# Kernel tuning notes

Measured on AMD Instinct MI355X. Metric: run time of the kernel, lower is better.

The kernel has to match this reference:

```python
import jax, jax.numpy as jnp
import numpy as np

N = 100000
E = 1600000
IN_C = 128
HID = 32
HEADS = 4
OUT_C = 16
G = 128
NEG_SLOPE = 0.2


def setup_inputs() -> dict:
    key = jax.random.key(0)
    ks = jax.random.split(key, 16)
    x = jax.random.normal(ks[0], (N, IN_C), dtype=jnp.float32)
    edge_index = jax.random.randint(ks[1], (2, E), 0, N, dtype=jnp.int64)
    batch = jnp.sort(jax.random.randint(ks[2], (N,), 0, G, dtype=jnp.int64))
    node_weights = jax.random.uniform(ks[3], (N, 1), dtype=jnp.float32)
    s = 1.0 / np.sqrt(IN_C)
    W1 = jax.random.uniform(ks[4], (IN_C, HEADS * HID), jnp.float32, -s, s)
    att_src1 = jax.random.uniform(ks[5], (HEADS, HID), jnp.float32, -s, s)
    att_dst1 = jax.random.uniform(ks[6], (HEADS, HID), jnp.float32, -s, s)
    b1 = jnp.zeros((HEADS * HID,), jnp.float32)
    s2 = 1.0 / np.sqrt(HEADS * HID)
    W2 = jax.random.uniform(ks[7], (HEADS * HID, HID), jnp.float32, -s2, s2)
    att_src2 = jax.random.uniform(ks[8], (1, HID), jnp.float32, -s2, s2)
    att_dst2 = jax.random.uniform(ks[9], (1, HID), jnp.float32, -s2, s2)
    b2 = jnp.zeros((HID,), jnp.float32)
    s3 = 1.0 / np.sqrt(HID)
    fcW = jax.random.uniform(ks[10], (HID, OUT_C), jnp.float32, -s3, s3)
    fcb = jax.random.uniform(ks[11], (OUT_C,), jnp.float32, -s3, s3)
    return {"x": x, "edge_index": edge_index, "batch": batch,
            "node_weights": node_weights,
            "W1": W1, "att_src1": att_src1, "att_dst1": att_dst1, "b1": b1,
            "W2": W2, "att_src2": att_src2, "att_dst2": att_dst2, "b2": b2,
            "fcW": fcW, "fcb": fcb}


def gat_conv(x, src, dst, W, att_src, att_dst, bias, heads, ch, concat):
    n = x.shape[0]
    h = (x @ W).reshape(n, heads, ch)                       # [N,H,C]
    a_src = jnp.sum(h * att_src[None], axis=-1)             # [N,H]
    a_dst = jnp.sum(h * att_dst[None], axis=-1)             # [N,H]
    e = jax.nn.leaky_relu(a_src[src] + a_dst[dst], NEG_SLOPE)  # [E,H]
    # segment softmax over incoming edges of each destination node
    e_max = jax.ops.segment_max(e, dst, num_segments=n)
    ex = jnp.exp(e - e_max[dst])
    denom = jax.ops.segment_sum(ex, dst, num_segments=n)
    alpha = ex / denom[dst]                                 # [E,H]
    msg = h[src] * alpha[..., None]                         # [E,H,C]
    out = jax.ops.segment_sum(msg, dst, num_segments=n)     # [N,H,C]
    if concat:
        out = out.reshape(n, heads * ch)
    else:
        out = out.mean(axis=1)
    return out + bias


def reference(x, edge_index, batch, node_weights,
              W1, att_src1, att_dst1, b1,
              W2, att_src2, att_dst2, b2,
              fcW, fcb):
    n = x.shape[0]
    # PyG GATConv adds self-loops by default
    loop = jnp.arange(n, dtype=edge_index.dtype)
    src = jnp.concatenate([edge_index[0], loop])
    dst = jnp.concatenate([edge_index[1], loop])

    h = x * node_weights
    h = jax.nn.elu(gat_conv(h, src, dst, W1, att_src1, att_dst1, b1, HEADS, HID, True))
    h = jax.nn.elu(gat_conv(h, src, dst, W2, att_src2, att_dst2, b2, 1, HID, False))
    # global mean pool over graphs
    sums = jax.ops.segment_sum(h, batch, num_segments=G)
    cnts = jax.ops.segment_sum(jnp.ones((n,), h.dtype), batch, num_segments=G)
    pooled = sums / jnp.maximum(cnts, 1.0)[:, None]
    return pooled @ fcW + fcb
```

## Files before the change

### kernel.cpp

```cpp
#include <hip/hip_runtime.h>
#include <cstdint>

#define OUT_C 16
#define NGRAPH 128
#define NEG 0.2f
#define NB_MAX 512
#define BSH 8
#define BSZ 256
#define CAP 8192

typedef unsigned int uint;
typedef unsigned short ushort;
typedef unsigned char uchar;
typedef __attribute__((ext_vector_type(8))) short bf16x8;
typedef __attribute__((ext_vector_type(4))) float f32x4;
typedef __attribute__((ext_vector_type(2))) float f32x2;

union U4B { uint4 u; bf16x8 v; };

__device__ __forceinline__ ushort f2bf(float f) {
  uint u = __float_as_uint(f);
  uint r = (u + 0x7FFF + ((u >> 16) & 1)) >> 16;
  return (ushort)r;
}

__device__ __forceinline__ int wave_incl_scan_i(int v) {
  int lane = threadIdx.x & 63;
#pragma unroll
  for (int off = 1; off < 64; off <<= 1) {
    int u = __shfl_up(v, off, 64);
    if (lane >= off) v += u;
  }
  return v;
}

__global__ void k_bin(const int* __restrict__ ei,
                      const float* __restrict__ W1, const float* __restrict__ W2,
                      ushort* __restrict__ Wt1, ushort* __restrict__ Wt2,
                      int E, int Etot, int NB, int nbin,
                      int* __restrict__ bcur, uint* __restrict__ bbuf) {
  if (blockIdx.x >= nbin) {
    int t2 = (blockIdx.x - nbin) * 256 + threadIdx.x;
    if (t2 < 16384) {
      int n = t2 >> 7, k = t2 & 127;
      Wt1[t2] = f2bf(W1[k * 128 + n]);
    } else {
      int u = t2 - 16384;
      int n = u >> 7, k = u & 127;
      Wt2[u] = f2bf(W2[k * 32 + n]);
    }
    return;
  }
  __shared__ int h[NB_MAX];
  __shared__ int baseo[NB_MAX];
  int t = threadIdx.x;
  for (int b = t; b < NB; b += 256) h[b] = 0;
  __syncthreads();
  int cbase = blockIdx.x * 4096;
  int cend = min(cbase + 4096, Etot);
  for (int e = cbase + t; e < cend; e += 256) {
    int d = (e < E) ? ei[E + e] : (e - E);
    atomicAdd(&h[d >> BSH], 1);
  }
  __syncthreads();
  for (int b = t; b < NB; b += 256) {
    int c = h[b];
    baseo[b] = c ? atomicAdd(&bcur[b], c) : 0;
    h[b] = 0;
  }
  __syncthreads();
  for (int e = cbase + t; e < cend; e += 256) {
    int s, d;
    if (e < E) { s = ei[e]; d = ei[E + e]; } else { s = e - E; d = s; }
    int b = d >> BSH;
    int r = atomicAdd(&h[b], 1);
    bbuf[(size_t)b * CAP + baseo[b] + r] = ((uint)(d & (BSZ - 1)) << 17) | (uint)s;
  }
}

__global__ void k_bg(const uint* __restrict__ bbuf, const int* __restrict__ bcur,
                     int NB, int N, int* __restrict__ offs, int* __restrict__ ssrc,
                     const float* __restrict__ x, const ushort* __restrict__ Wt,
                     const float* __restrict__ nw, const float* __restrict__ att_s,
                     const float* __restrict__ att_d, uchar* __restrict__ hb1,
                     float* __restrict__ asrc, float* __restrict__ adst) {
  __shared__ int sst[NB_MAX + 1];
  __shared__ int wsum2[4];
  __shared__ int deg[BSZ];
  if (blockIdx.x < (uint)NB) {
    int t = threadIdx.x, lane = t & 63, wid = t >> 6;
    int v0 = (2 * t < NB) ? bcur[2 * t] : 0;
    int v1 = (2 * t + 1 < NB) ? bcur[2 * t + 1] : 0;
    int s = v0 + v1;
    int sv = wave_incl_scan_i(s);
    if (lane == 63) wsum2[wid] = sv;
    deg[t] = 0;
    __syncthreads();
    if (t == 0) {
      int r = 0;
#pragma unroll
      for (int k = 0; k < 4; k++) { int x2 = wsum2[k]; wsum2[k] = r; r += x2; }
    }
    __syncthreads();
    int excl = wsum2[wid] + sv - s;
    sst[2 * t] = excl;
    sst[2 * t + 1] = excl + v0;
    if (t == 255) sst[512] = excl + v0 + v1;
    __syncthreads();
    int b = blockIdx.x;
    int ebeg = sst[b], eend = sst[b + 1];
    int cnt = eend - ebeg;
    for (int i = t; i < cnt; i += BSZ)
      atomicAdd(&deg[bbuf[(size_t)b * CAP + i] >> 17], 1);
    __syncthreads();
    int v = deg[t];
    int sv2 = wave_incl_scan_i(v);
    if (lane == 63) wsum2[wid] = sv2;
    __syncthreads();
    if (t == 0) {
      int r = 0;
#pragma unroll
      for (int k = 0; k < 4; k++) { int x2 = wsum2[k]; wsum2[k] = r; r += x2; }
    }
    __syncthreads();
    int excl2 = wsum2[wid] + sv2 - v;
    int node = (b << BSH) + t;
    if (node < N) offs[node] = ebeg + excl2;
    if (b == 0 && t == 0) offs[N] = sst[512];
    __syncthreads();
    deg[t] = excl2;
    __syncthreads();
    for (int i = t; i < cnt; i += BSZ) {
      uint rec = bbuf[(size_t)b * CAP + i];
      int r = atomicAdd(&deg[rec >> 17], 1);
      ssrc[ebeg + r] = (int)(rec & 0x1FFFF);
    }
    return;
  }
  int bid = blockIdx.x - NB;
  int wv = threadIdx.x >> 6, l = threadIdx.x & 63;
  int lg = l >> 4, lr = l & 15;
  int row0 = bid * 64 + wv * 16;
  int node = row0 + lr;
  bool valid = node < N;
  float sc = valid ? nw[node] : 0.f;
  bf16x8 xfr[4];
  const float* xr = x + (size_t)node * 128;
#pragma unroll
  for (int kc = 0; kc < 4; kc++) {
    float v[8];
    if (valid) {
      float4 q0 = *reinterpret_cast<const float4*>(xr + kc * 32 + lg * 8);
      float4 q1 = *reinterpret_cast<const float4*>(xr + kc * 32 + lg * 8 + 4);
      v[0] = q0.x; v[1] = q0.y; v[2] = q0.z; v[3] = q0.w;
      v[4] = q1.x; v[5] = q1.y; v[6] = q1.z; v[7] = q1.w;
    } else {
#pragma unroll
      for (int j = 0; j < 8; j++) v[j] = 0.f;
    }
    U4B a;
    uint pk0 = (uint)f2bf(v[0] * sc) | ((uint)f2bf(v[1] * sc) << 16);
    uint pk1 = (uint)f2bf(v[2] * sc) | ((uint)f2bf(v[3] * sc) << 16);
    uint pk2 = (uint)f2bf(v[4] * sc) | ((uint)f2bf(v[5] * sc) << 16);
    uint pk3 = (uint)f2bf(v[6] * sc) | ((uint)f2bf(v[7] * sc) << 16);
    a.u = make_uint4(pk0, pk1, pk2, pk3);
    xfr[kc] = a.v;
  }
  float pS[4] = {}, pD[4] = {};
#pragma unroll
  for (int ct = 0; ct < 8; ct++) {
    f32x4 acc = {0.f, 0.f, 0.f, 0.f};
    const ushort* wrow = Wt + (size_t)(ct * 16 + lr) * 128;
#pragma unroll
    for (int kc = 0; kc < 4; kc++) {
      U4B bfr;
      bfr.u = *reinterpret_cast<const uint4*>(wrow + kc * 32 + lg * 8);
      acc = __builtin_amdgcn_mfma_f32_16x16x32_bf16(bfr.v, xfr[kc], acc, 0, 0, 0);
    }
    int c0 = ct * 16 + lg * 4;
    if (valid) {
      uint u8 = (uint)__builtin_amdgcn_cvt_pk_fp8_f32(acc[0], acc[1], 0, false);
      u8 = (uint)__builtin_amdgcn_cvt_pk_fp8_f32(acc[2], acc[3], u8, true);
      *reinterpret_cast<uint*>(hb1 + (size_t)node * 128 + c0) = u8;
    }
    float4 as4 = *reinterpret_cast<const float4*>(att_s + c0);
    float4 ad4 = *reinterpret_cast<const float4*>(att_d + c0);
    int h = ct >> 1;
    pS[h] += acc[0] * as4.x + acc[1] * as4.y + acc[2] * as4.z + acc[3] * as4.w;
    pD[h] += acc[0] * ad4.x + acc[1] * ad4.y + acc[2] * ad4.z + acc[3] * ad4.w;
  }
#pragma unroll
  for (int off = 16; off < 64; off <<= 1) {
#pragma unroll
    for (int h = 0; h < 4; h++) {
      pS[h] += __shfl_xor(pS[h], off, 64);
      pD[h] += __shfl_xor(pD[h], off, 64);
    }
  }
  if (lg == 0 && valid) {
    *reinterpret_cast<float4*>(asrc + node * 4) = make_float4(pS[0], pS[1], pS[2], pS[3]);
    *reinterpret_cast<float4*>(adst + node * 4) = make_float4(pD[0], pD[1], pD[2], pD[3]);
  }
}

__global__ void k_gemm2(const ushort* __restrict__ A, const ushort* __restrict__ Wt,
                        const float* __restrict__ att_s, const float* __restrict__ att_d,
                        uchar* __restrict__ hb2, float* __restrict__ asrc,
                        float* __restrict__ adst, int M) {
  int wv = threadIdx.x >> 6, l = threadIdx.x & 63;
  int lg = l >> 4, lr = l & 15;
  int row0 = blockIdx.x * 64 + wv * 16;
  int node = row0 + lr;
  bool valid = node < M;
  bf16x8 afr[4];
#pragma unroll
  for (int kc = 0; kc < 4; kc++) {
    U4B a;
    if (valid) a.u = *reinterpret_cast<const uint4*>(A + (size_t)node * 128 + kc * 32 + lg * 8);
    else a.u = make_uint4(0, 0, 0, 0);
    afr[kc] = a.v;
  }
  float pS = 0.f, pD = 0.f;
#pragma unroll
  for (int ct = 0; ct < 2; ct++) {
    f32x4 acc = {0.f, 0.f, 0.f, 0.f};
    const ushort* wrow = Wt + (size_t)(ct * 16 + lr) * 128;
#pragma unroll
    for (int kc = 0; kc < 4; kc++) {
      U4B bfr;
      bfr.u = *reinterpret_cast<const uint4*>(wrow + kc * 32 + lg * 8);
      acc = __builtin_amdgcn_mfma_f32_16x16x32_bf16(bfr.v, afr[kc], acc, 0, 0, 0);
    }
    int c0 = ct * 16 + lg * 4;
    if (valid) {
      uint u8 = (uint)__builtin_amdgcn_cvt_pk_fp8_f32(acc[0], acc[1], 0, false);
      u8 = (uint)__builtin_amdgcn_cvt_pk_fp8_f32(acc[2], acc[3], u8, true);
      *reinterpret_cast<uint*>(hb2 + (size_t)node * 32 + c0) = u8;
    }
    float4 as4 = *reinterpret_cast<const float4*>(att_s + c0);
    float4 ad4 = *reinterpret_cast<const float4*>(att_d + c0);
    pS += acc[0] * as4.x + acc[1] * as4.y + acc[2] * as4.z + acc[3] * as4.w;
    pD += acc[0] * ad4.x + acc[1] * ad4.y + acc[2] * ad4.z + acc[3] * ad4.w;
  }
#pragma unroll
  for (int off = 16; off < 64; off <<= 1) {
    pS += __shfl_xor(pS, off, 64);
    pD += __shfl_xor(pD, off, 64);
  }
  if (lg == 0 && valid) { asrc[node] = pS; adst[node] = pD; }
}

__global__ void k_aggr1(const int* __restrict__ offs, const int* __restrict__ ssrc,
                        const uchar* __restrict__ hb, const float* __restrict__ asrc,
                        const float* __restrict__ adst, const float* __restrict__ bias,
                        ushort* __restrict__ outb, int N) {
  int wid = threadIdx.x >> 6, l = threadIdx.x & 63;
  int d = blockIdx.x * 4 + wid;
  if (d >= N) return;
  int slot = l >> 3;
  int k = l & 7;
  int h = k >> 1;
  float ad = adst[d * 4 + h];
  int beg = offs[d], end = offs[d + 1];
  float a[16] = {};
  float ds = 0.f;
  for (int i = beg; i < end; i += 8) {
    int e = i + slot;
    int ec = min(e, end - 1);
    int s = ssrc[ec];
    float xv = asrc[s * 4 + h] + ad;
    xv = xv > 0.f ? xv : NEG * xv;
    float w = __expf(xv);
    w = (e < end) ? w : 0.f;
    uint4 p = *reinterpret_cast<const uint4*>(hb + (size_t)s * 128 + k * 16);
    uint pu[4] = {p.x, p.y, p.z, p.w};
#pragma unroll
    for (int q = 0; q < 4; q++) {
      f32x2 f0 = __builtin_amdgcn_cvt_pk_f32_fp8(pu[q], false);
      f32x2 f1 = __builtin_amdgcn_cvt_pk_f32_fp8(pu[q], true);
      a[q * 4 + 0] += w * f0.x;
      a[q * 4 + 1] += w * f0.y;
      a[q * 4 + 2] += w * f1.x;
      a[q * 4 + 3] += w * f1.y;
    }
    ds += w;
  }
  int b3 = (l >> 3) & 1, b4 = (l >> 4) & 1, b5 = (l >> 5) & 1;
  float t8[8];
#pragma unroll
  for (int r = 0; r < 8; r++) {
    float send = b3 ? a[r] : a[r + 8];
    float recv = __shfl_xor(send, 8, 64);
    t8[r] = (b3 ? a[r + 8] : a[r]) + recv;
  }
  float t4[4];
#pragma unroll
  for (int r = 0; r < 4; r++) {
    float send = b4 ? t8[r] : t8[r + 4];
    float recv = __shfl_xor(send, 16, 64);
    t4[r] = (b4 ? t8[r + 4] : t8[r]) + recv;
  }
  float t2[2];
#pragma unroll
  for (int r = 0; r < 2; r++) {
    float send = b5 ? t4[r] : t4[r + 2];
    float recv = __shfl_xor(send, 32, 64);
    t2[r] = (b5 ? t4[r + 2] : t4[r]) + recv;
  }
  ds += __shfl_xor(ds, 8, 64);
  ds += __shfl_xor(ds, 16, 64);
  ds += __shfl_xor(ds, 32, 64);
  float inv = 1.f / ds;
  int c0 = k * 16 + b3 * 8 + b4 * 4 + b5 * 2;
  float r0 = t2[0] * inv + bias[c0];
  float r1 = t2[1] * inv + bias[c0 + 1];
  r0 = r0 > 0.f ? r0 : expm1f(r0);
  r1 = r1 > 0.f ? r1 : expm1f(r1);
  *reinterpret_cast<uint*>(outb + (size_t)d * 128 + c0) =
      (uint)f2bf(r0) | ((uint)f2bf(r1) << 16);
}

__global__ void k_aggr2(const int* __restrict__ offs, const int* __restrict__ ssrc,
                        const uchar* __restrict__ hb, const float* __restrict__ asrc,
                        const float* __restrict__ adst, const float* __restrict__ bias,
                        float* __restrict__ out, int N) {
  int wid = threadIdx.x >> 6, l = threadIdx.x & 63;
  int d = blockIdx.x * 4 + wid;
  if (d >= N) return;
  int slot = l >> 2;
  int k = l & 3;
  float ad = adst[d];
  int beg = offs[d], end = offs[d + 1];
  float a[8] = {};
  float ds = 0.f;
  for (int i = beg; i < end; i += 16) {
    int e = i + slot;
    int ec = min(e, end - 1);
    int s = ssrc[ec];
    float xv = asrc[s] + ad;
    xv = xv > 0.f ? xv : NEG * xv;
    float w = __expf(xv);
    w = (e < end) ? w : 0.f;
    uint2 p = *reinterpret_cast<const uint2*>(hb + (size_t)s * 32 + k * 8);
    f32x2 f0 = __builtin_amdgcn_cvt_pk_f32_fp8(p.x, false);
    f32x2 f1 = __builtin_amdgcn_cvt_pk_f32_fp8(p.x, true);
    f32x2 f2 = __builtin_amdgcn_cvt_pk_f32_fp8(p.y, false);
    f32x2 f3 = __builtin_amdgcn_cvt_pk_f32_fp8(p.y, true);
    a[0] += w * f0.x; a[1] += w * f0.y; a[2] += w * f1.x; a[3] += w * f1.y;
    a[4] += w * f2.x; a[5] += w * f2.y; a[6] += w * f3.x; a[7] += w * f3.y;
    ds += w;
  }
  int b2 = (l >> 2) & 1, b3 = (l >> 3) & 1, b4 = (l >> 4) & 1;
  float t4[4];
#pragma unroll
  for (int r = 0; r < 4; r++) {
    float send = b2 ? a[r] : a[r + 4];
    float recv = __shfl_xor(send, 4, 64);
    t4[r] = (b2 ? a[r + 4] : a[r]) + recv;
  }
  float t2[2];
#pragma unroll
  for (int r = 0; r < 2; r++) {
    float send = b3 ? t4[r] : t4[r + 2];
    float recv = __shfl_xor(send, 8, 64);
    t2[r] = (b3 ? t4[r + 2] : t4[r]) + recv;
  }
  float send = b4 ? t2[0] : t2[1];
  float recv = __shfl_xor(send, 16, 64);
  float t1 = (b4 ? t2[1] : t2[0]) + recv;
  t1 += __shfl_xor(t1, 32, 64);
  ds += __shfl_xor(ds, 4, 64);
  ds += __shfl_xor(ds, 8, 64);
  ds += __shfl_xor(ds, 16, 64);
  ds += __shfl_xor(ds, 32, 64);
  if (l < 32) {
    int c = k * 8 + b2 * 4 + b3 * 2 + b4;
    float r = t1 / ds + bias[c];
    r = r > 0.f ? r : expm1f(r);
    out[(size_t)d * 32 + c] = r;
  }
}

__global__ void k_pool_fc(const float* __restrict__ h2, const int* __restrict__ batch,
                          const float* __restrict__ fcW, const float* __restrict__ fcb,
                          float* __restrict__ out, int N) {
  int g = blockIdx.x;
  int lo = 0, hi = N;
  while (lo < hi) { int mid = (lo + hi) >> 1; if (batch[mid] < g) lo = mid + 1; else hi = mid; }
  int beg = lo;
  hi = N;
  while (lo < hi) { int mid = (lo + hi) >> 1; if (batch[mid] < g + 1) lo = mid + 1; else hi = mid; }
  int end = lo;
  int t = threadIdx.x, c = t & 31, sub = t >> 5;
  float acc = 0.f;
  for (int n = beg + sub; n < end; n += 8) acc += h2[(size_t)n * 32 + c];
  __shared__ float red[8][32];
  __shared__ float pooled[32];
  red[sub][c] = acc;
  __syncthreads();
  if (sub == 0) {
    float s = 0.f;
#pragma unroll
    for (int i = 0; i < 8; i++) s += red[i][c];
    float cnt = (float)(end - beg);
    pooled[c] = s / fmaxf(cnt, 1.f);
  }
  __syncthreads();
  if (t < 16) {
    float r = fcb[t];
#pragma unroll
    for (int cc = 0; cc < 32; cc++) r += pooled[cc] * fcW[cc * 16 + t];
    out[g * 16 + t] = r;
  }
}

extern "C" void kernel_launch(void* const* d_in, const int* in_sizes, int n_in,
                              void* d_out, int out_size, void* d_ws, size_t ws_size,
                              hipStream_t stream) {
  const float* x     = (const float*)d_in[0];
  const int*   ei    = (const int*)d_in[1];
  const int*   batch = (const int*)d_in[2];
  const float* nw    = (const float*)d_in[3];
  const float* W1    = (const float*)d_in[4];
  const float* as1w  = (const float*)d_in[5];
  const float* ad1w  = (const float*)d_in[6];
  const float* b1    = (const float*)d_in[7];
  const float* W2    = (const float*)d_in[8];
  const float* as2w  = (const float*)d_in[9];
  const float* ad2w  = (const float*)d_in[10];
  const float* b2    = (const float*)d_in[11];
  const float* fcW   = (const float*)d_in[12];
  const float* fcb   = (const float*)d_in[13];
  float* out = (float*)d_out;

  const int N = in_sizes[0] / 128;
  const int E = in_sizes[1] / 2;
  const int Etot = E + N;
  const int NB = (N + BSZ - 1) >> BSH;

  char* w = (char*)d_ws;
  size_t ofs = 0;
  auto alloc = [&](size_t bytes) {
    char* p = w + ofs;
    ofs += (bytes + 255) & ~(size_t)255;
    return p;
  };
  uchar*  hb1    = (uchar*)alloc((size_t)N * 128);
  ushort* out1b  = (ushort*)alloc((size_t)N * 128 * 2);
  uchar*  hb2    = (uchar*)alloc((size_t)N * 32);
  float*  h2     = (float*)alloc((size_t)N * 32 * 4);
  float*  asrc1  = (float*)alloc((size_t)N * 4 * 4);
  float*  adst1  = (float*)alloc((size_t)N * 4 * 4);
  float*  asrc2  = (float*)alloc((size_t)N * 4);
  float*  adst2  = (float*)alloc((size_t)N * 4);
  ushort* Wt1    = (ushort*)alloc(16384 * 2);
  ushort* Wt2    = (ushort*)alloc(4096 * 2);
  int*    bcur   = (int*)alloc((size_t)NB * 4);
  int*    offs   = (int*)alloc((size_t)(N + 1) * 4);
  uint*   bbuf   = (uint*)alloc((size_t)NB * CAP * 4);
  int*    ssrc   = (int*)alloc((size_t)Etot * 4);

  hipMemsetAsync(bcur, 0, (size_t)NB * 4, stream);

  const int nbin = (Etot + 4095) / 4096;
  k_bin<<<nbin + 80, 256, 0, stream>>>(ei, W1, W2, Wt1, Wt2, E, Etot, NB, nbin, bcur, bbuf);

  const int ngemm1 = (N + 63) / 64;
  k_bg<<<NB + ngemm1, 256, 0, stream>>>(bbuf, bcur, NB, N, offs, ssrc,
                                        x, Wt1, nw, as1w, ad1w, hb1, asrc1, adst1);

  k_aggr1<<<(N + 3) / 4, 256, 0, stream>>>(offs, ssrc, hb1, asrc1, adst1, b1, out1b, N);

  k_gemm2<<<(N + 63) / 64, 256, 0, stream>>>(out1b, Wt2, as2w, ad2w, hb2, asrc2, adst2, N);
  k_aggr2<<<(N + 3) / 4, 256, 0, stream>>>(offs, ssrc, hb2, asrc2, adst2, b2, h2, N);

  k_pool_fc<<<NGRAPH, 256, 0, stream>>>(h2, batch, fcW, fcb, out, N);
}
```

Before: 314.3 us.

## Fuse layer-2 linear projection and attention logits into layer-1 aggregation kernel

Removes the separate MFMA GEMM kernel for layer 2. The layer-1 aggregation kernel now stages the fp32 W2 matrix in shared memory and computes each node's 32-channel projection with scalar FMAs after the ELU. It then writes the fp8 features and the src/dst attention scalars directly, which drops the bf16 intermediate buffer write/read and one kernel launch. The aggregation loop is also unrolled to process two edges per lane per iteration. In exchange, every block reloads 16KB of W2 into LDS, the extra LDS use may reduce occupancy, and the projection no longer uses MFMA.

```diff
diff --git a/kernel.cpp b/kernel.cpp
--- a/kernel.cpp
+++ b/kernel.cpp
@@ -35,20 +35,13 @@
 }
 
 __global__ void k_bin(const int* __restrict__ ei,
-                      const float* __restrict__ W1, const float* __restrict__ W2,
-                      ushort* __restrict__ Wt1, ushort* __restrict__ Wt2,
+                      const float* __restrict__ W1, ushort* __restrict__ Wt1,
                       int E, int Etot, int NB, int nbin,
                       int* __restrict__ bcur, uint* __restrict__ bbuf) {
-  if (blockIdx.x >= nbin) {
+  if (blockIdx.x >= (uint)nbin) {
     int t2 = (blockIdx.x - nbin) * 256 + threadIdx.x;
-    if (t2 < 16384) {
-      int n = t2 >> 7, k = t2 & 127;
-      Wt1[t2] = f2bf(W1[k * 128 + n]);
-    } else {
-      int u = t2 - 16384;
-      int n = u >> 7, k = u & 127;
-      Wt2[u] = f2bf(W2[k * 32 + n]);
-    }
+    int n = t2 >> 7, k = t2 & 127;
+    Wt1[t2] = f2bf(W1[k * 128 + n]);
     return;
   }
   __shared__ int h[NB_MAX];
@@ -203,68 +196,56 @@
   }
 }
 
-__global__ void k_gemm2(const ushort* __restrict__ A, const ushort* __restrict__ Wt,
-                        const float* __restrict__ att_s, const float* __restrict__ att_d,
-                        uchar* __restrict__ hb2, float* __restrict__ asrc,
-                        float* __restrict__ adst, int M) {
-  int wv = threadIdx.x >> 6, l = threadIdx.x & 63;
-  int lg = l >> 4, lr = l & 15;
-  int row0 = blockIdx.x * 64 + wv * 16;
-  int node = row0 + lr;
-  bool valid = node < M;
-  bf16x8 afr[4];
-#pragma unroll
-  for (int kc = 0; kc < 4; kc++) {
-    U4B a;
-    if (valid) a.u = *reinterpret_cast<const uint4*>(A + (size_t)node * 128 + kc * 32 + lg * 8);
-    else a.u = make_uint4(0, 0, 0, 0);
-    afr[kc] = a.v;
-  }
-  float pS = 0.f, pD = 0.f;
-#pragma unroll
-  for (int ct = 0; ct < 2; ct++) {
-    f32x4 acc = {0.f, 0.f, 0.f, 0.f};
-    const ushort* wrow = Wt + (size_t)(ct * 16 + lr) * 128;
-#pragma unroll
-    for (int kc = 0; kc < 4; kc++) {
-      U4B bfr;
-      bfr.u = *reinterpret_cast<const uint4*>(wrow + kc * 32 + lg * 8);
-      acc = __builtin_amdgcn_mfma_f32_16x16x32_bf16(bfr.v, afr[kc], acc, 0, 0, 0);
-    }
-    int c0 = ct * 16 + lg * 4;
-    if (valid) {
-      uint u8 = (uint)__builtin_amdgcn_cvt_pk_fp8_f32(acc[0], acc[1], 0, false);
-      u8 = (uint)__builtin_amdgcn_cvt_pk_fp8_f32(acc[2], acc[3], u8, true);
-      *reinterpret_cast<uint*>(hb2 + (size_t)node * 32 + c0) = u8;
-    }
-    float4 as4 = *reinterpret_cast<const float4*>(att_s + c0);
-    float4 ad4 = *reinterpret_cast<const float4*>(att_d + c0);
-    pS += acc[0] * as4.x + acc[1] * as4.y + acc[2] * as4.z + acc[3] * as4.w;
-    pD += acc[0] * ad4.x + acc[1] * ad4.y + acc[2] * ad4.z + acc[3] * ad4.w;
-  }
-#pragma unroll
-  for (int off = 16; off < 64; off <<= 1) {
-    pS += __shfl_xor(pS, off, 64);
-    pD += __shfl_xor(pD, off, 64);
-  }
-  if (lg == 0 && valid) { asrc[node] = pS; adst[node] = pD; }
-}
-
 __global__ void k_aggr1(const int* __restrict__ offs, const int* __restrict__ ssrc,
                         const uchar* __restrict__ hb, const float* __restrict__ asrc,
                         const float* __restrict__ adst, const float* __restrict__ bias,
-                        ushort* __restrict__ outb, int N) {
-  int wid = threadIdx.x >> 6, l = threadIdx.x & 63;
+                        const float* __restrict__ W2, const float* __restrict__ as2,
+                        const float* __restrict__ ad2, uchar* __restrict__ hb2,
+                        float* __restrict__ asrc2, float* __restrict__ adst2, int N) {
+  __shared__ float W2s[128 * 32];
+  __shared__ float rowl[4][128];
+  int tid = threadIdx.x;
+#pragma unroll
+  for (int q = 0; q < 4; q++) {
+    int idx = (tid + q * 256) * 4;
+    *reinterpret_cast<float4*>(&W2s[idx]) = *reinterpret_cast<const float4*>(W2 + idx);
+  }
+  __syncthreads();
+  int wid = tid >> 6, l = tid & 63;
   int d = blockIdx.x * 4 + wid;
   if (d >= N) return;
   int slot = l >> 3;
-  int k = l & 7;
-  int h = k >> 1;
+  int cb = l & 7;
+  int h = cb >> 1;
   float ad = adst[d * 4 + h];
   int beg = offs[d], end = offs[d + 1];
   float a[16] = {};
   float ds = 0.f;
-  for (int i = beg; i < end; i += 8) {
+  int i = beg;
+  for (; i + 16 <= end; i += 16) {
+    int s0 = ssrc[i + slot];
+    int s1 = ssrc[i + 8 + slot];
+    uint4 p0 = *reinterpret_cast<const uint4*>(hb + (size_t)s0 * 128 + cb * 16);
+    uint4 p1 = *reinterpret_cast<const uint4*>(hb + (size_t)s1 * 128 + cb * 16);
+    float x0 = asrc[s0 * 4 + h] + ad; x0 = x0 > 0.f ? x0 : NEG * x0;
+    float x1 = asrc[s1 * 4 + h] + ad; x1 = x1 > 0.f ? x1 : NEG * x1;
+    float w0 = __expf(x0), w1 = __expf(x1);
+    uint pu0[4] = {p0.x, p0.y, p0.z, p0.w};
+    uint pu1[4] = {p1.x, p1.y, p1.z, p1.w};
+#pragma unroll
+    for (int q = 0; q < 4; q++) {
+      f32x2 g0 = __builtin_amdgcn_cvt_pk_f32_fp8(pu0[q], false);
+      f32x2 g1 = __builtin_amdgcn_cvt_pk_f32_fp8(pu0[q], true);
+      f32x2 g2 = __builtin_amdgcn_cvt_pk_f32_fp8(pu1[q], false);
+      f32x2 g3 = __builtin_amdgcn_cvt_pk_f32_fp8(pu1[q], true);
+      a[q * 4 + 0] += w0 * g0.x + w1 * g2.x;
+      a[q * 4 + 1] += w0 * g0.y + w1 * g2.y;
+      a[q * 4 + 2] += w0 * g1.x + w1 * g3.x;
+      a[q * 4 + 3] += w0 * g1.y + w1 * g3.y;
+    }
+    ds += w0 + w1;
+  }
+  for (; i < end; i += 8) {
     int e = i + slot;
     int ec = min(e, end - 1);
     int s = ssrc[ec];
@@ -272,7 +253,7 @@
     xv = xv > 0.f ? xv : NEG * xv;
     float w = __expf(xv);
     w = (e < end) ? w : 0.f;
-    uint4 p = *reinterpret_cast<const uint4*>(hb + (size_t)s * 128 + k * 16);
+    uint4 p = *reinterpret_cast<const uint4*>(hb + (size_t)s * 128 + cb * 16);
     uint pu[4] = {p.x, p.y, p.z, p.w};
 #pragma unroll
     for (int q = 0; q < 4; q++) {
@@ -311,13 +292,33 @@
   ds += __shfl_xor(ds, 16, 64);
   ds += __shfl_xor(ds, 32, 64);
   float inv = 1.f / ds;
-  int c0 = k * 16 + b3 * 8 + b4 * 4 + b5 * 2;
+  int c0 = cb * 16 + b3 * 8 + b4 * 4 + b5 * 2;
   float r0 = t2[0] * inv + bias[c0];
   float r1 = t2[1] * inv + bias[c0 + 1];
   r0 = r0 > 0.f ? r0 : expm1f(r0);
   r1 = r1 > 0.f ? r1 : expm1f(r1);
-  *reinterpret_cast<uint*>(outb + (size_t)d * 128 + c0) =
-      (uint)f2bf(r0) | ((uint)f2bf(r1) << 16);
+  rowl[wid][c0] = r0;
+  rowl[wid][c0 + 1] = r1;
+  int c = l & 31, half = l >> 5;
+  int kb = half * 64;
+  float acc2 = 0.f;
+#pragma unroll
+  for (int k2 = 0; k2 < 64; k2 += 2) {
+    float2 rv = *reinterpret_cast<const float2*>(&rowl[wid][kb + k2]);
+    acc2 += rv.x * W2s[(kb + k2) * 32 + c] + rv.y * W2s[(kb + k2 + 1) * 32 + c];
+  }
+  acc2 += __shfl_xor(acc2, 32, 64);
+  if (half == 0) {
+    uint b8 = (uint)__builtin_amdgcn_cvt_pk_fp8_f32(acc2, acc2, 0, false);
+    hb2[(size_t)d * 32 + c] = (uchar)(b8 & 0xFF);
+    float ps = acc2 * as2[c], pd = acc2 * ad2[c];
+#pragma unroll
+    for (int off = 1; off < 32; off <<= 1) {
+      ps += __shfl_xor(ps, off, 32);
+      pd += __shfl_xor(pd, off, 32);
+    }
+    if (c == 0) { asrc2[d] = ps; adst2[d] = pd; }
+  }
 }
 
 __global__ void k_aggr2(const int* __restrict__ offs, const int* __restrict__ ssrc,
@@ -446,7 +447,6 @@
     return p;
   };
   uchar*  hb1    = (uchar*)alloc((size_t)N * 128);
-  ushort* out1b  = (ushort*)alloc((size_t)N * 128 * 2);
   uchar*  hb2    = (uchar*)alloc((size_t)N * 32);
   float*  h2     = (float*)alloc((size_t)N * 32 * 4);
   float*  asrc1  = (float*)alloc((size_t)N * 4 * 4);
@@ -454,7 +454,6 @@
   float*  asrc2  = (float*)alloc((size_t)N * 4);
   float*  adst2  = (float*)alloc((size_t)N * 4);
   ushort* Wt1    = (ushort*)alloc(16384 * 2);
-  ushort* Wt2    = (ushort*)alloc(4096 * 2);
   int*    bcur   = (int*)alloc((size_t)NB * 4);
   int*    offs   = (int*)alloc((size_t)(N + 1) * 4);
   uint*   bbuf   = (uint*)alloc((size_t)NB * CAP * 4);
@@ -463,15 +462,15 @@
   hipMemsetAsync(bcur, 0, (size_t)NB * 4, stream);
 
   const int nbin = (Etot + 4095) / 4096;
-  k_bin<<<nbin + 80, 256, 0, stream>>>(ei, W1, W2, Wt1, Wt2, E, Etot, NB, nbin, bcur, bbuf);
+  k_bin<<<nbin + 64, 256, 0, stream>>>(ei, W1, Wt1, E, Etot, NB, nbin, bcur, bbuf);
 
   const int ngemm1 = (N + 63) / 64;
   k_bg<<<NB + ngemm1, 256, 0, stream>>>(bbuf, bcur, NB, N, offs, ssrc,
                                         x, Wt1, nw, as1w, ad1w, hb1, asrc1, adst1);
 
-  k_aggr1<<<(N + 3) / 4, 256, 0, stream>>>(offs, ssrc, hb1, asrc1, adst1, b1, out1b, N);
-
-  k_gemm2<<<(N + 63) / 64, 256, 0, stream>>>(out1b, Wt2, as2w, ad2w, hb2, asrc2, adst2, N);
+  k_aggr1<<<(N + 3) / 4, 256, 0, stream>>>(offs, ssrc, hb1, asrc1, adst1, b1,
+                                           W2, as2w, ad2w, hb2, asrc2, adst2, N);
+
   k_aggr2<<<(N + 3) / 4, 256, 0, stream>>>(offs, ssrc, hb2, asrc2, adst2, b2, h2, N);
 
   k_pool_fc<<<NGRAPH, 256, 0, stream>>>(h2, batch, fcW, fcb, out, N);
```

After: 330.2 us. 1.05x slower.

## Fuse layer-2 linear transform and attention logits into layer-1 aggregation kernel

Applied to the files above, without the earlier changes.

The layer-1 aggregation kernel now writes its bf16 output rows for its 4 destination nodes into shared memory. After a block barrier, wave 0 runs the 128x32 MFMA projection, fp8-packs hb2 and computes the layer-2 attention logits, so the separate k_gemm2 launch goes away. This removes the global write and read of the N x 128 bf16 intermediate and one kernel launch. In exchange, three of four waves idle during the GEMM tail, each block adds a barrier, and the 16x16 MFMA tile is only a quarter used (4 real rows).

```diff
diff --git a/kernel.cpp b/kernel.cpp
--- a/kernel.cpp
+++ b/kernel.cpp
@@ -1,7 +1,6 @@
 #include <hip/hip_runtime.h>
 #include <cstdint>
 
-#define OUT_C 16
 #define NGRAPH 128
 #define NEG 0.2f
 #define NB_MAX 512
@@ -39,7 +38,7 @@
                       ushort* __restrict__ Wt1, ushort* __restrict__ Wt2,
                       int E, int Etot, int NB, int nbin,
                       int* __restrict__ bcur, uint* __restrict__ bbuf) {
-  if (blockIdx.x >= nbin) {
+  if (blockIdx.x >= (uint)nbin) {
     int t2 = (blockIdx.x - nbin) * 256 + threadIdx.x;
     if (t2 < 16384) {
       int n = t2 >> 7, k = t2 & 127;
@@ -203,65 +202,22 @@
   }
 }
 
-__global__ void k_gemm2(const ushort* __restrict__ A, const ushort* __restrict__ Wt,
-                        const float* __restrict__ att_s, const float* __restrict__ att_d,
-                        uchar* __restrict__ hb2, float* __restrict__ asrc,
-                        float* __restrict__ adst, int M) {
-  int wv = threadIdx.x >> 6, l = threadIdx.x & 63;
-  int lg = l >> 4, lr = l & 15;
-  int row0 = blockIdx.x * 64 + wv * 16;
-  int node = row0 + lr;
-  bool valid = node < M;
-  bf16x8 afr[4];
-#pragma unroll
-  for (int kc = 0; kc < 4; kc++) {
-    U4B a;
-    if (valid) a.u = *reinterpret_cast<const uint4*>(A + (size_t)node * 128 + kc * 32 + lg * 8);
-    else a.u = make_uint4(0, 0, 0, 0);
-    afr[kc] = a.v;
-  }
-  float pS = 0.f, pD = 0.f;
-#pragma unroll
-  for (int ct = 0; ct < 2; ct++) {
-    f32x4 acc = {0.f, 0.f, 0.f, 0.f};
-    const ushort* wrow = Wt + (size_t)(ct * 16 + lr) * 128;
-#pragma unroll
-    for (int kc = 0; kc < 4; kc++) {
-      U4B bfr;
-      bfr.u = *reinterpret_cast<const uint4*>(wrow + kc * 32 + lg * 8);
-      acc = __builtin_amdgcn_mfma_f32_16x16x32_bf16(bfr.v, afr[kc], acc, 0, 0, 0);
-    }
-    int c0 = ct * 16 + lg * 4;
-    if (valid) {
-      uint u8 = (uint)__builtin_amdgcn_cvt_pk_fp8_f32(acc[0], acc[1], 0, false);
-      u8 = (uint)__builtin_amdgcn_cvt_pk_fp8_f32(acc[2], acc[3], u8, true);
-      *reinterpret_cast<uint*>(hb2 + (size_t)node * 32 + c0) = u8;
-    }
-    float4 as4 = *reinterpret_cast<const float4*>(att_s + c0);
-    float4 ad4 = *reinterpret_cast<const float4*>(att_d + c0);
-    pS += acc[0] * as4.x + acc[1] * as4.y + acc[2] * as4.z + acc[3] * as4.w;
-    pD += acc[0] * ad4.x + acc[1] * ad4.y + acc[2] * ad4.z + acc[3] * ad4.w;
-  }
-#pragma unroll
-  for (int off = 16; off < 64; off <<= 1) {
-    pS += __shfl_xor(pS, off, 64);
-    pD += __shfl_xor(pD, off, 64);
-  }
-  if (lg == 0 && valid) { asrc[node] = pS; adst[node] = pD; }
-}
-
 __global__ void k_aggr1(const int* __restrict__ offs, const int* __restrict__ ssrc,
                         const uchar* __restrict__ hb, const float* __restrict__ asrc,
                         const float* __restrict__ adst, const float* __restrict__ bias,
-                        ushort* __restrict__ outb, int N) {
-  int wid = threadIdx.x >> 6, l = threadIdx.x & 63;
-  int d = blockIdx.x * 4 + wid;
-  if (d >= N) return;
+                        const ushort* __restrict__ Wt2, const float* __restrict__ as2,
+                        const float* __restrict__ ad2, uchar* __restrict__ hb2,
+                        float* __restrict__ asrc2, float* __restrict__ adst2, int N) {
+  __shared__ ushort rowl[4][136];
+  int tid = threadIdx.x;
+  int wv = tid >> 6, l = tid & 63;
+  int d = blockIdx.x * 4 + wv;
+  int dc = min(d, N - 1);
   int slot = l >> 3;
-  int k = l & 7;
-  int h = k >> 1;
-  float ad = adst[d * 4 + h];
-  int beg = offs[d], end = offs[d + 1];
+  int cb = l & 7;
+  int h = cb >> 1;
+  float ad = adst[dc * 4 + h];
+  int beg = offs[dc], end = offs[dc + 1];
   float a[16] = {};
   float ds = 0.f;
   for (int i = beg; i < end; i += 8) {
@@ -272,7 +228,7 @@
     xv = xv > 0.f ? xv : NEG * xv;
     float w = __expf(xv);
     w = (e < end) ? w : 0.f;
-    uint4 p = *reinterpret_cast<const uint4*>(hb + (size_t)s * 128 + k * 16);
+    uint4 p = *reinterpret_cast<const uint4*>(hb + (size_t)s * 128 + cb * 16);
     uint pu[4] = {p.x, p.y, p.z, p.w};
 #pragma unroll
     for (int q = 0; q < 4; q++) {
@@ -310,14 +266,53 @@
   ds += __shfl_xor(ds, 8, 64);
   ds += __shfl_xor(ds, 16, 64);
   ds += __shfl_xor(ds, 32, 64);
-  float inv = 1.f / ds;
-  int c0 = k * 16 + b3 * 8 + b4 * 4 + b5 * 2;
+  float inv = 1.f / (ds > 0.f ? ds : 1.f);
+  int c0 = cb * 16 + b3 * 8 + b4 * 4 + b5 * 2;
   float r0 = t2[0] * inv + bias[c0];
   float r1 = t2[1] * inv + bias[c0 + 1];
   r0 = r0 > 0.f ? r0 : expm1f(r0);
   r1 = r1 > 0.f ? r1 : expm1f(r1);
-  *reinterpret_cast<uint*>(outb + (size_t)d * 128 + c0) =
-      (uint)f2bf(r0) | ((uint)f2bf(r1) << 16);
+  *reinterpret_cast<uint*>(&rowl[wv][c0]) = (uint)f2bf(r0) | ((uint)f2bf(r1) << 16);
+  __syncthreads();
+  if (wv != 0) return;
+  int lg = l >> 4, lr = l & 15;
+  int rsel = lr & 3;
+  bf16x8 bfrag[4];
+#pragma unroll
+  for (int kc = 0; kc < 4; kc++) {
+    U4B bb;
+    bb.u = *reinterpret_cast<const uint4*>(&rowl[rsel][kc * 32 + lg * 8]);
+    bfrag[kc] = bb.v;
+  }
+  int dd = blockIdx.x * 4 + lr;
+  bool vs = (lr < 4) && (dd < N);
+  float pS = 0.f, pD = 0.f;
+#pragma unroll
+  for (int ct = 0; ct < 2; ct++) {
+    f32x4 acc = {0.f, 0.f, 0.f, 0.f};
+    const ushort* wrow = Wt2 + (size_t)(ct * 16 + lr) * 128;
+#pragma unroll
+    for (int kc = 0; kc < 4; kc++) {
+      U4B bfr;
+      bfr.u = *reinterpret_cast<const uint4*>(wrow + kc * 32 + lg * 8);
+      acc = __builtin_amdgcn_mfma_f32_16x16x32_bf16(bfr.v, bfrag[kc], acc, 0, 0, 0);
+    }
+    int cg = ct * 16 + lg * 4;
+    if (vs) {
+      uint u8 = (uint)__builtin_amdgcn_cvt_pk_fp8_f32(acc[0], acc[1], 0, false);
+      u8 = (uint)__builtin_amdgcn_cvt_pk_fp8_f32(acc[2], acc[3], u8, true);
+      *reinterpret_cast<uint*>(hb2 + (size_t)dd * 32 + cg) = u8;
+    }
+    float4 as4 = *reinterpret_cast<const float4*>(as2 + cg);
+    float4 ad4 = *reinterpret_cast<const float4*>(ad2 + cg);
+    pS += acc[0] * as4.x + acc[1] * as4.y + acc[2] * as4.z + acc[3] * as4.w;
+    pD += acc[0] * ad4.x + acc[1] * ad4.y + acc[2] * ad4.z + acc[3] * ad4.w;
+  }
+  pS += __shfl_xor(pS, 16, 64);
+  pS += __shfl_xor(pS, 32, 64);
+  pD += __shfl_xor(pD, 16, 64);
+  pD += __shfl_xor(pD, 32, 64);
+  if (vs && lg == 0) { asrc2[dd] = pS; adst2[dd] = pD; }
 }
 
 __global__ void k_aggr2(const int* __restrict__ offs, const int* __restrict__ ssrc,
@@ -446,7 +441,6 @@
     return p;
   };
   uchar*  hb1    = (uchar*)alloc((size_t)N * 128);
-  ushort* out1b  = (ushort*)alloc((size_t)N * 128 * 2);
   uchar*  hb2    = (uchar*)alloc((size_t)N * 32);
   float*  h2     = (float*)alloc((size_t)N * 32 * 4);
   float*  asrc1  = (float*)alloc((size_t)N * 4 * 4);
@@ -469,9 +463,9 @@
   k_bg<<<NB + ngemm1, 256, 0, stream>>>(bbuf, bcur, NB, N, offs, ssrc,
                                         x, Wt1, nw, as1w, ad1w, hb1, asrc1, adst1);
 
-  k_aggr1<<<(N + 3) / 4, 256, 0, stream>>>(offs, ssrc, hb1, asrc1, adst1, b1, out1b, N);
-
-  k_gemm2<<<(N + 63) / 64, 256, 0, stream>>>(out1b, Wt2, as2w, ad2w, hb2, asrc2, adst2, N);
+  k_aggr1<<<(N + 3) / 4, 256, 0, stream>>>(offs, ssrc, hb1, asrc1, adst1, b1,
+                                           Wt2, as2w, ad2w, hb2, asrc2, adst2, N);
+
   k_aggr2<<<(N + 3) / 4, 256, 0, stream>>>(offs, ssrc, hb2, asrc2, adst2, b2, h2, N);
 
   k_pool_fc<<<NGRAPH, 256, 0, stream>>>(h2, batch, fcW, fcb, out, N);
```

After: 312.2 us (median of 2 runs). About the same (-0.7%).
